# Performance work log

Hardware: AMD Instinct MI355X
Metric: run time of the kernel (lower is better)

The kernel has to match this reference:

```python
import jax, jax.numpy as jnp
import numpy as np

B, S, D = 4, 2048, 1024
H, DK = 16, 64

def setup_inputs() -> dict:
    key = jax.random.key(0)
    ks = jax.random.split(key, 11)
    s_in = 1.0 / np.sqrt(D)      # torch Linear default init scale ~ U(-1/sqrt(fan_in),..)
    s_out = 1.0 / np.sqrt(H * DK)
    return {
        "q_in": jax.random.normal(ks[0], (B, S, D), jnp.float32),
        "k_in": jax.random.normal(ks[1], (B, S, D), jnp.float32),
        "v_in": jax.random.normal(ks[2], (B, S, D), jnp.float32),
        # per-head projection weights, stacked over heads: [H, D, DK]
        "wq": jax.random.uniform(ks[3], (H, D, DK), jnp.float32, -s_in, s_in),
        "bq": jax.random.uniform(ks[4], (H, DK), jnp.float32, -s_in, s_in),
        "wk": jax.random.uniform(ks[5], (H, D, DK), jnp.float32, -s_in, s_in),
        "bk": jax.random.uniform(ks[6], (H, DK), jnp.float32, -s_in, s_in),
        "wv": jax.random.uniform(ks[7], (H, D, DK), jnp.float32, -s_in, s_in),
        "bv": jax.random.uniform(ks[8], (H, DK), jnp.float32, -s_in, s_in),
        # output linear: [H*DK, D]
        "wo": jax.random.uniform(ks[9], (H * DK, D), jnp.float32, -s_out, s_out),
        "bo": jax.random.uniform(ks[10], (D,), jnp.float32, -s_out, s_out),
    }

def reference(q_in, k_in, v_in, wq, bq, wk, bk, wv, bv, wo, bo):
    # per-head projections, batched over heads: [B,H,S,DK]
    q = jnp.einsum("bsd,hdk->bhsk", q_in, wq) + bq[None, :, None, :]
    k = jnp.einsum("bsd,hdk->bhsk", k_in, wk) + bk[None, :, None, :]
    v = jnp.einsum("bsd,hdk->bhsk", v_in, wv) + bv[None, :, None, :]
    scale = q.shape[-1] ** 0.5
    scores = jnp.einsum("bhsk,bhtk->bhst", q, k) / scale  # [B,H,S,S]
    attn = jax.nn.softmax(scores, axis=-1)
    out = jnp.einsum("bhst,bhtk->bhsk", attn, v)           # [B,H,S,DK]
    # concat heads along last dim (head-major order matches torch.cat over heads)
    cat = jnp.transpose(out, (0, 2, 1, 3)).reshape(B, S, H * DK)
    return cat @ wo + bo
```

## Files before the change

### kernel.cpp

```cpp
#include <hip/hip_runtime.h>
#include <hip/hip_bf16.h>
#include <math.h>

typedef short bf16x8 __attribute__((ext_vector_type(8)));
typedef unsigned short us8 __attribute__((ext_vector_type(8)));
typedef unsigned short us4 __attribute__((ext_vector_type(4)));
typedef float f32x2 __attribute__((ext_vector_type(2)));
typedef float f32x4 __attribute__((ext_vector_type(4)));
typedef float f32x16 __attribute__((ext_vector_type(16)));
typedef unsigned int u32;
typedef unsigned int u32x4 __attribute__((ext_vector_type(4)));

__device__ __forceinline__ unsigned short f2bf(float f) {
  unsigned int u = __builtin_bit_cast(unsigned int, f);
  u += 0x7fffu + ((u >> 16) & 1u);
  return (unsigned short)(u >> 16);
}

__device__ __forceinline__ void gload16(const void* g, void* l) {
  __builtin_amdgcn_global_load_lds(
      (const __attribute__((address_space(1))) unsigned int*)g,
      (__attribute__((address_space(3))) unsigned int*)l, 16, 0, 0);
}

__global__ __launch_bounds__(256) void k_conv3(const float* __restrict__ i0,
                                               const float* __restrict__ i1,
                                               const float* __restrict__ i2,
                                               unsigned short* __restrict__ o0,
                                               unsigned short* __restrict__ o1,
                                               unsigned short* __restrict__ o2) {
  int bid = blockIdx.x;
  int g = bid >> 13;
  const float* in = g == 0 ? i0 : g == 1 ? i1 : i2;
  unsigned short* out = g == 0 ? o0 : g == 1 ? o1 : o2;
  int i = (bid & 8191) * 256 + threadIdx.x;
  float4 v = ((const float4*)in)[i];
  us4 o;
  o[0] = f2bf(v.x); o[1] = f2bf(v.y); o[2] = f2bf(v.z); o[3] = f2bf(v.w);
  ((us4*)out)[i] = o;
}

__global__ __launch_bounds__(256) void k_pack4(const float* __restrict__ wq,
                                               const float* __restrict__ wk,
                                               const float* __restrict__ wv,
                                               const float* __restrict__ wo,
                                               unsigned short* __restrict__ Wqt,
                                               unsigned short* __restrict__ Wkt,
                                               unsigned short* __restrict__ Wvt,
                                               unsigned short* __restrict__ Wot) {
  __shared__ float tl[64][65];
  int bid = blockIdx.x;
  int g = bid >> 8;
  int bl = bid & 255;
  int tid = threadIdx.x;
  if (g < 3) {
    const float* w = g == 0 ? wq : g == 1 ? wk : wv;
    unsigned short* wt = g == 0 ? Wqt : g == 1 ? Wkt : Wvt;
    int h = bl >> 4, dt = bl & 15;
#pragma unroll
    for (int i = 0; i < 16; ++i) {
      int idx = i * 256 + tid;
      int d = idx >> 6, c = idx & 63;
      tl[c][d] = w[h * 65536 + (dt * 64 + d) * 64 + c];
    }
    __syncthreads();
#pragma unroll
    for (int i = 0; i < 16; ++i) {
      int idx = i * 256 + tid;
      int c = idx >> 6, d = idx & 63;
      wt[(h * 64 + c) * 1024 + dt * 64 + d] = f2bf(tl[c][d]);
    }
  } else {
    int kt = bl >> 4, nt = bl & 15;
#pragma unroll
    for (int i = 0; i < 16; ++i) {
      int idx = i * 256 + tid;
      int k = idx >> 6, n = idx & 63;
      tl[n][k] = wo[(kt * 64 + k) * 1024 + nt * 64 + n];
    }
    __syncthreads();
#pragma unroll
    for (int i = 0; i < 16; ++i) {
      int idx = i * 256 + tid;
      int n = idx >> 6, k = idx & 63;
      Wot[(nt * 64 + n) * 1024 + kt * 64 + k] = f2bf(tl[n][k]);
    }
  }
}

template<int OUT_BF16>
__device__ __forceinline__ void gemm_body(const unsigned short* __restrict__ A,
                                          const unsigned short* __restrict__ Bt,
                                          const float* __restrict__ bias,
                                          void* __restrict__ Cout, float scale,
                                          int bid) {
  __shared__ unsigned short As[2][128 * 32];
  __shared__ unsigned short Bs[2][128 * 32];
  const int tid = threadIdx.x;
  const int l = tid & 63, w = tid >> 6;
  const int wr = w >> 1, wc = w & 1;
  bid = (bid & 7) * 64 + (bid >> 3);
  const int bx = bid & 7;
  const int by = bid >> 3;
  const long brow = (long)by * 128;
  const int bcol = bx * 128;
  const int lr = l & 15, lg = l >> 4;
  f32x4 acc[4][4] = {};

  const char* aS0 = (const char*)(A + (brow + (tid >> 2)) * 1024 + (tid & 3) * 8);
  const char* aS1 = aS0 + 131072;
  const char* bS0 = (const char*)(Bt + (long)(bcol + (tid >> 2)) * 1024 + (tid & 3) * 8);
  const char* bS1 = bS0 + 131072;
  char* aD = (char*)&As[0][0] + w * 1024;
  char* bD = (char*)&Bs[0][0] + w * 1024;
  const char* aP = (const char*)&As[0][0] + ((wr * 64 + lr) * 32 + lg * 8) * 2;
  const char* bP = (const char*)&Bs[0][0] + ((wc * 64 + lr) * 32 + lg * 8) * 2;

  auto stage = [&](int curbuf) {
    gload16(aS0, aD + curbuf * 8192);
    gload16(aS1, aD + curbuf * 8192 + 4096);
    gload16(bS0, bD + curbuf * 8192);
    gload16(bS1, bD + curbuf * 8192 + 4096);
    aS0 += 64; aS1 += 64; bS0 += 64; bS1 += 64;
  };

  stage(0);
  for (int kk = 0; kk < 16; ++kk) {
#pragma unroll
    for (int cur = 0; cur < 2; ++cur) {
      int k0 = kk * 64 + cur * 32;
      __syncthreads();
      if (k0 + 32 < 1024) stage(cur ^ 1);
      bf16x8 af[4], bfr[4];
#pragma unroll
      for (int m = 0; m < 4; ++m)
        af[m] = *(const bf16x8*)(aP + cur * 8192 + m * 1024);
#pragma unroll
      for (int n = 0; n < 4; ++n)
        bfr[n] = *(const bf16x8*)(bP + cur * 8192 + n * 1024);
#pragma unroll
      for (int m = 0; m < 4; ++m)
#pragma unroll
        for (int n = 0; n < 4; ++n)
          acc[m][n] = __builtin_amdgcn_mfma_f32_16x16x32_bf16(af[m], bfr[n], acc[m][n], 0, 0, 0);
    }
  }

#pragma unroll
  for (int m = 0; m < 4; ++m) {
#pragma unroll
    for (int n = 0; n < 4; ++n) {
      int col = bcol + wc * 64 + n * 16 + lr;
      float bia = bias[col];
#pragma unroll
      for (int i = 0; i < 4; ++i) {
        long row = brow + wr * 64 + m * 16 + lg * 4 + i;
        float v = (acc[m][n][i] + bia) * scale;
        if (OUT_BF16) ((unsigned short*)Cout)[row * 1024 + col] = f2bf(v);
        else          ((float*)Cout)[row * 1024 + col] = v;
      }
    }
  }
}

__global__ __launch_bounds__(256) void k_gemm_qkv(const unsigned short* __restrict__ Aq,
                                                  const unsigned short* __restrict__ Ak,
                                                  const unsigned short* __restrict__ Av,
                                                  const unsigned short* __restrict__ Wqt,
                                                  const unsigned short* __restrict__ Wkt,
                                                  const unsigned short* __restrict__ Wvt,
                                                  const float* __restrict__ bq,
                                                  const float* __restrict__ bk,
                                                  const float* __restrict__ bv,
                                                  unsigned short* __restrict__ Qa,
                                                  unsigned short* __restrict__ Ka,
                                                  unsigned short* __restrict__ Va,
                                                  float qscale) {
  int g = blockIdx.x >> 9;
  int bl = blockIdx.x & 511;
  const unsigned short* A  = g == 0 ? Aq  : g == 1 ? Ak  : Av;
  const unsigned short* Bt = g == 0 ? Wqt : g == 1 ? Wkt : Wvt;
  const float* bia         = g == 0 ? bq  : g == 1 ? bk  : bv;
  unsigned short* C        = g == 0 ? Qa  : g == 1 ? Ka  : Va;
  gemm_body<1>(A, Bt, bia, C, g == 0 ? qscale : 1.0f, bl);
}

__global__ __launch_bounds__(256) void k_gemm_wo(const unsigned short* __restrict__ A,
                                                 const unsigned short* __restrict__ Bt,
                                                 const float* __restrict__ bias,
                                                 float* __restrict__ Cout) {
  gemm_body<0>(A, Bt, bias, Cout, 1.0f, blockIdx.x);
}

__global__ __launch_bounds__(256) void k_transpose_v(const unsigned short* __restrict__ V,
                                                     unsigned short* __restrict__ Vt) {
  __shared__ unsigned short tile[64][72];
  int bid = blockIdx.x;
  int bh = bid >> 5, st = bid & 31;
  int b = bh >> 4, h = bh & 15;
  int tid = threadIdx.x;
#pragma unroll
  for (int i = 0; i < 2; ++i) {
    int idx = i * 256 + tid;
    int r = idx >> 3, ch = idx & 7;
    us8 v = *(const us8*)&V[((long)(b * 2048 + st * 64 + r)) * 1024 + h * 64 + ch * 8];
#pragma unroll
    for (int j = 0; j < 8; ++j) tile[ch * 8 + j][r] = v[j];
  }
  __syncthreads();
#pragma unroll
  for (int i = 0; i < 2; ++i) {
    int idx = i * 256 + tid;
    int c = idx >> 3, ch = idx & 7;
    us8 v;
#pragma unroll
    for (int j = 0; j < 8; ++j) v[j] = tile[c][ch * 8 + j];
    *(us8*)&Vt[(long)bh * 131072 + (long)c * 2048 + st * 64 + ch * 8] = v;
  }
}

__global__ __launch_bounds__(256) void k_attn4(const unsigned short* __restrict__ Q,
                                               const unsigned short* __restrict__ K,
                                               const unsigned short* __restrict__ Vt,
                                               unsigned short* __restrict__ AO) {
  __shared__ unsigned short KV[4][4096];
  __shared__ float Li[4][32];
  const int tid = threadIdx.x;
  const int l = tid & 63, w = tid >> 6;
  const int l31 = l & 31, hi = l >> 5;
  int bid0 = blockIdx.x;
  int bid = (bid0 & 7) * 128 + (bid0 >> 3);
  const int bh = bid >> 4, qt0 = bid & 15;
  const int b = bh >> 4, h = bh & 15;
  const unsigned short* Qb = Q + (long)b * 2048 * 1024 + h * 64;
  const unsigned short* Kb = K + (long)b * 2048 * 1024 + h * 64;
  const unsigned short* Vb = Vt + (long)bh * 131072;
  const int qbase = qt0 * 128 + w * 32;

  bf16x8 qf[4];
#pragma unroll
  for (int c = 0; c < 4; ++c)
    qf[c] = *(const bf16x8*)&Qb[(long)(qbase + l31) * 1024 + c * 16 + hi * 8];

  f32x16 acc[2] = {};
  f32x16 z16 = {};
  f32x2 li2a = {0.f, 0.f}, li2b = {0.f, 0.f};
  const int rsw = (l31 & 7) << 4;

  const char* pb[4];
#pragma unroll
  for (int c = 0; c < 4; ++c)
    pb[c] = (const char*)&KV[0][0] + l31 * 128 + ((c * 32 + hi * 16) ^ rsw);

  const int sch = tid & 7, srw = tid >> 3;
  const int ssw = (sch * 16) ^ ((srw & 7) << 4);
  const char* ks0 = (const char*)Kb + (long)srw * 2048 + ssw;
  const char* ks1 = ks0 + 65536;
  const char* vs0 = (const char*)Vb + (long)srw * 4096 + ssw;
  const char* vs1 = vs0 + 131072;
  char* dK = (char*)&KV[0][0] + w * 1024;
  char* dV = dK + 8192;

  auto stage = [&](int buf) {
    gload16(ks0, dK + buf * 16384);
    gload16(ks1, dK + buf * 16384 + 4096);
    gload16(vs0, dV + buf * 16384);
    gload16(vs1, dV + buf * 16384 + 4096);
    ks0 += 131072; ks1 += 131072;
    vs0 += 128;    vs1 += 128;
  };

  stage(0);
  for (int it = 0; it < 16; ++it) {
#pragma unroll
    for (int cur = 0; cur < 2; ++cur) {
      __syncthreads();
      if (it < 15 || cur == 0) stage(cur ^ 1);

      bf16x8 paf[4];
#pragma unroll
      for (int h2 = 0; h2 < 2; ++h2) {
        bf16x8 kf[4];
#pragma unroll
        for (int c = 0; c < 4; ++c)
          kf[c] = *(const bf16x8*)(pb[c] + cur * 16384 + h2 * 4096);
        f32x16 s = __builtin_amdgcn_mfma_f32_32x32x16_bf16(kf[0], qf[0], z16, 0, 0, 0);
#pragma unroll
        for (int c = 1; c < 4; ++c)
          s = __builtin_amdgcn_mfma_f32_32x32x16_bf16(kf[c], qf[c], s, 0, 0, 0);
        float p[16];
#pragma unroll
        for (int r = 0; r < 16; ++r) p[r] = __builtin_amdgcn_exp2f(s[r]);
#pragma unroll
        for (int g = 0; g < 4; ++g) {
          f32x2 pa; pa[0] = p[4 * g]; pa[1] = p[4 * g + 1];
          f32x2 pc; pc[0] = p[4 * g + 2]; pc[1] = p[4 * g + 3];
          li2a += pa; li2b += pc;
        }
        u32 wg[4][2];
#pragma unroll
        for (int g = 0; g < 4; ++g) {
          asm("v_cvt_pk_bf16_f32 %0, %1, %2" : "=v"(wg[g][0]) : "v"(p[4 * g]), "v"(p[4 * g + 1]));
          asm("v_cvt_pk_bf16_f32 %0, %1, %2" : "=v"(wg[g][1]) : "v"(p[4 * g + 2]), "v"(p[4 * g + 3]));
        }
#pragma unroll
        for (int sub = 0; sub < 2; ++sub) {
          u32 x0 = wg[2 * sub][0], y0 = wg[2 * sub + 1][0];
          u32 x1 = wg[2 * sub][1], y1 = wg[2 * sub + 1][1];
          asm("v_permlane32_swap_b32 %0, %1" : "+v"(x0), "+v"(y0));
          asm("v_permlane32_swap_b32 %0, %1" : "+v"(x1), "+v"(y1));
          u32x4 fw; fw[0] = x0; fw[1] = x1; fw[2] = y0; fw[3] = y1;
          paf[h2 * 2 + sub] = __builtin_bit_cast(bf16x8, fw);
        }
      }
#pragma unroll
      for (int ck = 0; ck < 4; ++ck)
#pragma unroll
        for (int ct = 0; ct < 2; ++ct) {
          bf16x8 vf = *(const bf16x8*)(pb[ck] + cur * 16384 + 8192 + ct * 4096);
          acc[ct] = __builtin_amdgcn_mfma_f32_32x32x16_bf16(paf[ck], vf, acc[ct], 0, 0, 0);
        }
    }
  }

  float li = li2a[0] + li2a[1] + li2b[0] + li2b[1];
  li += __shfl_xor(li, 32);
  if (hi == 0) Li[w][l31] = 1.f / li;
#pragma unroll
  for (int ct = 0; ct < 2; ++ct)
#pragma unroll
    for (int r = 0; r < 16; ++r) {
      int qrow = (r & 3) + 8 * (r >> 2) + 4 * hi;
      float inv = Li[w][qrow];
      long row = (long)b * 2048 + qbase + qrow;
      int col = h * 64 + ct * 32 + l31;
      AO[row * 1024 + col] = f2bf(acc[ct][r] * inv);
    }
}

extern "C" void kernel_launch(void* const* d_in, const int* in_sizes, int n_in,
                              void* d_out, int out_size, void* d_ws, size_t ws_size,
                              hipStream_t stream) {
  (void)in_sizes; (void)n_in; (void)out_size; (void)ws_size;
  const float* q_in = (const float*)d_in[0];
  const float* k_in = (const float*)d_in[1];
  const float* v_in = (const float*)d_in[2];
  const float* wq   = (const float*)d_in[3];
  const float* bq   = (const float*)d_in[4];
  const float* wk   = (const float*)d_in[5];
  const float* bk   = (const float*)d_in[6];
  const float* wv   = (const float*)d_in[7];
  const float* bv   = (const float*)d_in[8];
  const float* wo   = (const float*)d_in[9];
  const float* bo   = (const float*)d_in[10];

  char* ws = (char*)d_ws;
  const size_t SZA = (size_t)8192 * 1024 * 2;
  unsigned short* Aq  = (unsigned short*)(ws);
  unsigned short* Ak  = (unsigned short*)(ws + SZA);
  unsigned short* Av  = (unsigned short*)(ws + 2 * SZA);
  unsigned short* Qa  = (unsigned short*)(ws + 3 * SZA);
  unsigned short* Ka  = (unsigned short*)(ws + 4 * SZA);
  unsigned short* Va  = (unsigned short*)(ws + 5 * SZA);
  unsigned short* Wqt = (unsigned short*)(ws + 6 * SZA);
  unsigned short* Wkt = Wqt + 1048576;
  unsigned short* Wvt = Wkt + 1048576;
  unsigned short* Wot = Wvt + 1048576;
  unsigned short* Vtr = Ak;
  unsigned short* AO  = Aq;

  const float QSCALE = 0.1803368801111204f;

  k_conv3<<<24576, 256, 0, stream>>>(q_in, k_in, v_in, Aq, Ak, Av);
  k_pack4<<<1024, 256, 0, stream>>>(wq, wk, wv, wo, Wqt, Wkt, Wvt, Wot);
  k_gemm_qkv<<<1536, 256, 0, stream>>>(Aq, Ak, Av, Wqt, Wkt, Wvt, bq, bk, bv,
                                       Qa, Ka, Va, QSCALE);
  k_transpose_v<<<2048, 256, 0, stream>>>(Va, Vtr);
  k_attn4<<<1024, 256, 0, stream>>>(Qa, Ka, Vtr, AO);
  k_gemm_wo<<<512, 256, 0, stream>>>(AO, Wot, bo, (float*)d_out);
}
```

Baseline: 357.6 us.

## Process 64 query rows per wave in attention to reuse K/V fragments

Each wave in the attention kernel now handles two 32-row query sub-tiles instead of one, so every K and V fragment read from LDS feeds twice as many MFMAs. The block covers 256 query rows and the grid shrinks from 1024 to 512 blocks. The aim is to halve LDS traffic and global K/V staging per unit of compute. In exchange each wave holds more accumulators and register fragments, and there are fewer blocks to spread over the CUs, which may reduce occupancy.

```diff
diff --git a/kernel.cpp b/kernel.cpp
--- a/kernel.cpp
+++ b/kernel.cpp
@@ -219,32 +219,35 @@
   }
 }
 
-__global__ __launch_bounds__(256) void k_attn4(const unsigned short* __restrict__ Q,
+__global__ __launch_bounds__(256) void k_attn6(const unsigned short* __restrict__ Q,
                                                const unsigned short* __restrict__ K,
                                                const unsigned short* __restrict__ Vt,
                                                unsigned short* __restrict__ AO) {
   __shared__ unsigned short KV[4][4096];
-  __shared__ float Li[4][32];
+  __shared__ float Li[4][64];
   const int tid = threadIdx.x;
   const int l = tid & 63, w = tid >> 6;
   const int l31 = l & 31, hi = l >> 5;
   int bid0 = blockIdx.x;
-  int bid = (bid0 & 7) * 128 + (bid0 >> 3);
-  const int bh = bid >> 4, qt0 = bid & 15;
+  int bid = (bid0 & 7) * 64 + (bid0 >> 3);
+  const int bh = bid >> 3, qt0 = bid & 7;
   const int b = bh >> 4, h = bh & 15;
   const unsigned short* Qb = Q + (long)b * 2048 * 1024 + h * 64;
   const unsigned short* Kb = K + (long)b * 2048 * 1024 + h * 64;
   const unsigned short* Vb = Vt + (long)bh * 131072;
-  const int qbase = qt0 * 128 + w * 32;
-
-  bf16x8 qf[4];
-#pragma unroll
-  for (int c = 0; c < 4; ++c)
-    qf[c] = *(const bf16x8*)&Qb[(long)(qbase + l31) * 1024 + c * 16 + hi * 8];
-
-  f32x16 acc[2] = {};
+  const int qbase = qt0 * 256 + w * 64;
+
+  bf16x8 qf0[4], qf1[4];
+#pragma unroll
+  for (int c = 0; c < 4; ++c) {
+    qf0[c] = *(const bf16x8*)&Qb[(long)(qbase + l31) * 1024 + c * 16 + hi * 8];
+    qf1[c] = *(const bf16x8*)&Qb[(long)(qbase + 32 + l31) * 1024 + c * 16 + hi * 8];
+  }
+
+  f32x16 acc00 = {}, acc01 = {}, acc10 = {}, acc11 = {};
   f32x16 z16 = {};
-  f32x2 li2a = {0.f, 0.f}, li2b = {0.f, 0.f};
+  f32x2 liA0 = {0.f, 0.f}, liB0 = {0.f, 0.f};
+  f32x2 liA1 = {0.f, 0.f}, liB1 = {0.f, 0.f};
   const int rsw = (l31 & 7) << 4;
 
   const char* pb[4];
@@ -277,64 +280,82 @@
       __syncthreads();
       if (it < 15 || cur == 0) stage(cur ^ 1);
 
-      bf16x8 paf[4];
 #pragma unroll
       for (int h2 = 0; h2 < 2; ++h2) {
         bf16x8 kf[4];
 #pragma unroll
         for (int c = 0; c < 4; ++c)
           kf[c] = *(const bf16x8*)(pb[c] + cur * 16384 + h2 * 4096);
-        f32x16 s = __builtin_amdgcn_mfma_f32_32x32x16_bf16(kf[0], qf[0], z16, 0, 0, 0);
-#pragma unroll
-        for (int c = 1; c < 4; ++c)
-          s = __builtin_amdgcn_mfma_f32_32x32x16_bf16(kf[c], qf[c], s, 0, 0, 0);
-        float p[16];
-#pragma unroll
-        for (int r = 0; r < 16; ++r) p[r] = __builtin_amdgcn_exp2f(s[r]);
-#pragma unroll
-        for (int g = 0; g < 4; ++g) {
-          f32x2 pa; pa[0] = p[4 * g]; pa[1] = p[4 * g + 1];
-          f32x2 pc; pc[0] = p[4 * g + 2]; pc[1] = p[4 * g + 3];
-          li2a += pa; li2b += pc;
+        f32x16 s0 = __builtin_amdgcn_mfma_f32_32x32x16_bf16(kf[0], qf0[0], z16, 0, 0, 0);
+        f32x16 s1 = __builtin_amdgcn_mfma_f32_32x32x16_bf16(kf[0], qf1[0], z16, 0, 0, 0);
+#pragma unroll
+        for (int c = 1; c < 4; ++c) {
+          s0 = __builtin_amdgcn_mfma_f32_32x32x16_bf16(kf[c], qf0[c], s0, 0, 0, 0);
+          s1 = __builtin_amdgcn_mfma_f32_32x32x16_bf16(kf[c], qf1[c], s1, 0, 0, 0);
         }
-        u32 wg[4][2];
-#pragma unroll
-        for (int g = 0; g < 4; ++g) {
-          asm("v_cvt_pk_bf16_f32 %0, %1, %2" : "=v"(wg[g][0]) : "v"(p[4 * g]), "v"(p[4 * g + 1]));
-          asm("v_cvt_pk_bf16_f32 %0, %1, %2" : "=v"(wg[g][1]) : "v"(p[4 * g + 2]), "v"(p[4 * g + 3]));
+        bf16x8 pa0[2], pa1[2];
+#pragma unroll
+        for (int qs = 0; qs < 2; ++qs) {
+          const f32x16& s = qs == 0 ? s0 : s1;
+          float p[16];
+#pragma unroll
+          for (int r = 0; r < 16; ++r) p[r] = __builtin_amdgcn_exp2f(s[r]);
+#pragma unroll
+          for (int g = 0; g < 4; ++g) {
+            f32x2 pa; pa[0] = p[4 * g]; pa[1] = p[4 * g + 1];
+            f32x2 pc; pc[0] = p[4 * g + 2]; pc[1] = p[4 * g + 3];
+            if (qs == 0) { liA0 += pa; liB0 += pc; }
+            else         { liA1 += pa; liB1 += pc; }
+          }
+          u32 wg[4][2];
+#pragma unroll
+          for (int g = 0; g < 4; ++g) {
+            asm("v_cvt_pk_bf16_f32 %0, %1, %2" : "=v"(wg[g][0]) : "v"(p[4 * g]), "v"(p[4 * g + 1]));
+            asm("v_cvt_pk_bf16_f32 %0, %1, %2" : "=v"(wg[g][1]) : "v"(p[4 * g + 2]), "v"(p[4 * g + 3]));
+          }
+#pragma unroll
+          for (int sub = 0; sub < 2; ++sub) {
+            u32 x0 = wg[2 * sub][0], y0 = wg[2 * sub + 1][0];
+            u32 x1 = wg[2 * sub][1], y1 = wg[2 * sub + 1][1];
+            asm("v_permlane32_swap_b32 %0, %1" : "+v"(x0), "+v"(y0));
+            asm("v_permlane32_swap_b32 %0, %1" : "+v"(x1), "+v"(y1));
+            u32x4 fw; fw[0] = x0; fw[1] = x1; fw[2] = y0; fw[3] = y1;
+            if (qs == 0) pa0[sub] = __builtin_bit_cast(bf16x8, fw);
+            else         pa1[sub] = __builtin_bit_cast(bf16x8, fw);
+          }
         }
 #pragma unroll
-        for (int sub = 0; sub < 2; ++sub) {
-          u32 x0 = wg[2 * sub][0], y0 = wg[2 * sub + 1][0];
-          u32 x1 = wg[2 * sub][1], y1 = wg[2 * sub + 1][1];
-          asm("v_permlane32_swap_b32 %0, %1" : "+v"(x0), "+v"(y0));
-          asm("v_permlane32_swap_b32 %0, %1" : "+v"(x1), "+v"(y1));
-          u32x4 fw; fw[0] = x0; fw[1] = x1; fw[2] = y0; fw[3] = y1;
-          paf[h2 * 2 + sub] = __builtin_bit_cast(bf16x8, fw);
+        for (int k2 = 0; k2 < 2; ++k2) {
+          const int ck = h2 * 2 + k2;
+          bf16x8 vf0 = *(const bf16x8*)(pb[ck] + cur * 16384 + 8192);
+          bf16x8 vf1 = *(const bf16x8*)(pb[ck] + cur * 16384 + 8192 + 4096);
+          acc00 = __builtin_amdgcn_mfma_f32_32x32x16_bf16(pa0[k2], vf0, acc00, 0, 0, 0);
+          acc01 = __builtin_amdgcn_mfma_f32_32x32x16_bf16(pa0[k2], vf1, acc01, 0, 0, 0);
+          acc10 = __builtin_amdgcn_mfma_f32_32x32x16_bf16(pa1[k2], vf0, acc10, 0, 0, 0);
+          acc11 = __builtin_amdgcn_mfma_f32_32x32x16_bf16(pa1[k2], vf1, acc11, 0, 0, 0);
         }
       }
-#pragma unroll
-      for (int ck = 0; ck < 4; ++ck)
-#pragma unroll
-        for (int ct = 0; ct < 2; ++ct) {
-          bf16x8 vf = *(const bf16x8*)(pb[ck] + cur * 16384 + 8192 + ct * 4096);
-          acc[ct] = __builtin_amdgcn_mfma_f32_32x32x16_bf16(paf[ck], vf, acc[ct], 0, 0, 0);
-        }
-    }
-  }
-
-  float li = li2a[0] + li2a[1] + li2b[0] + li2b[1];
-  li += __shfl_xor(li, 32);
-  if (hi == 0) Li[w][l31] = 1.f / li;
-#pragma unroll
-  for (int ct = 0; ct < 2; ++ct)
-#pragma unroll
-    for (int r = 0; r < 16; ++r) {
-      int qrow = (r & 3) + 8 * (r >> 2) + 4 * hi;
-      float inv = Li[w][qrow];
-      long row = (long)b * 2048 + qbase + qrow;
-      int col = h * 64 + ct * 32 + l31;
-      AO[row * 1024 + col] = f2bf(acc[ct][r] * inv);
+    }
+  }
+
+  float li0 = liA0[0] + liA0[1] + liB0[0] + liB0[1];
+  float li1 = liA1[0] + liA1[1] + liB1[0] + liB1[1];
+  li0 += __shfl_xor(li0, 32);
+  li1 += __shfl_xor(li1, 32);
+  if (hi == 0) { Li[w][l31] = 1.f / li0; Li[w][32 + l31] = 1.f / li1; }
+#pragma unroll
+  for (int qs = 0; qs < 2; ++qs)
+#pragma unroll
+    for (int ct = 0; ct < 2; ++ct) {
+      const f32x16& a = qs == 0 ? (ct == 0 ? acc00 : acc01) : (ct == 0 ? acc10 : acc11);
+#pragma unroll
+      for (int r = 0; r < 16; ++r) {
+        int qrow = (r & 3) + 8 * (r >> 2) + 4 * hi;
+        float inv = Li[w][qs * 32 + qrow];
+        long row = (long)b * 2048 + qbase + qs * 32 + qrow;
+        int col = h * 64 + ct * 32 + l31;
+        AO[row * 1024 + col] = f2bf(a[r] * inv);
+      }
     }
 }
 
@@ -376,6 +397,6 @@
   k_gemm_qkv<<<1536, 256, 0, stream>>>(Aq, Ak, Av, Wqt, Wkt, Wvt, bq, bk, bv,
                                        Qa, Ka, Va, QSCALE);
   k_transpose_v<<<2048, 256, 0, stream>>>(Va, Vtr);
-  k_attn4<<<1024, 256, 0, stream>>>(Qa, Ka, Vtr, AO);
+  k_attn6<<<512, 256, 0, stream>>>(Qa, Ka, Vtr, AO);
   k_gemm_wo<<<512, 256, 0, stream>>>(AO, Wot, bo, (float*)d_out);
 }
```

New measurement: 362.6 us. No clear change (+1.4%).
